# Kernel optimization log

Measured on AMD Instinct MI355X. Metric: run time of the kernel, lower is better.

The kernel has to match this reference:

```python
import jax, jax.numpy as jnp
import numpy as np

B, N_INST, C, K, H, W = 4, 64, 16, 4, 480, 480


def setup_inputs() -> dict:
    key = jax.random.key(0)
    k1, k2 = jax.random.split(key)
    # one binary-ish channel per instance, values in [0,1]
    update_map = jax.random.uniform(k1, (B, N_INST, H, W), dtype=jnp.float32)
    # current global instance-ID map, one channel per semantic category
    init_instance_map = jax.random.randint(k2, (B, C, H, W), 0, 50).astype(jnp.int32)
    # instance channel indices grouped by category (category c owns K instances)
    instance_ids = jnp.broadcast_to(
        jnp.arange(C * K, dtype=jnp.int32).reshape(C, K), (B, C, K)
    )
    return {
        "update_map": update_map,
        "init_instance_map": init_instance_map,
        "instance_ids": instance_ids,
    }


def reference(update_map, init_instance_map, instance_ids):
    b, n_inst, h, w = update_map.shape
    _, c, k = instance_ids.shape
    L = n_inst + 1  # local IDs live in [0, n_inst]
    BIG = jnp.int32(2 ** 30)

    # ---- aggregate instance channels per category (one-hot collapse) ----
    # gather the K instance channels of each category: [B, C, K, H, W]
    oh = jnp.take_along_axis(
        update_map[:, None, :, :, :],
        instance_ids[:, :, :, None, None].astype(jnp.int32),
        axis=2,
    )
    bg = jnp.full((b, c, 1, h, w), 1e-5, update_map.dtype)  # background plane
    idx = jnp.argmax(jnp.concatenate([bg, oh], axis=2), axis=2)  # [B, C, H, W]
    # remap argmax index -> instance ID via [0] + instance_ids
    padded_ids = jnp.concatenate(
        [jnp.zeros((b, c, 1), jnp.int32), instance_ids.astype(jnp.int32)], axis=2
    )  # [B, C, K+1]
    agg = padded_ids[
        jnp.arange(b)[:, None, None, None],
        jnp.arange(c)[None, :, None, None],
        idx,
    ]  # [B, C, H, W] local instance-ID map per category

    # ---- merge local IDs into global map, per env, sequential over categories ----
    def merge_env(gmap0, agg_e):
        def step(gmap, ci):
            local = agg_e[ci].reshape(-1)
            glob = gmap[ci].reshape(-1)
            max_id = jnp.max(gmap)  # max over ALL categories so far (sequential dep)
            # smallest overlapping nonzero global ID per local ID (torch.unique()[0])
            overlap_min = jax.ops.segment_min(
                jnp.where(glob != 0, glob, BIG), local, num_segments=L
            )
            present = jax.ops.segment_sum(
                jnp.ones_like(local), local, num_segments=L
            ) > 0
            has_overlap = overlap_min < BIG
            is_new = (present & (~has_overlap)).at[0].set(False)
            new_id = max_id + jnp.cumsum(is_new.astype(jnp.int32))
            mapping = jnp.where(has_overlap, overlap_min, jnp.where(is_new, new_id, 0))
            mapping = mapping.at[0].set(0)
            new_glob = jnp.maximum(glob, mapping[local]).reshape(h, w)
            updated = jnp.where(jnp.sum(agg_e[ci]) > 0, new_glob, gmap[ci])
            return gmap.at[ci].set(updated), None

        gmap, _ = jax.lax.scan(step, gmap0, jnp.arange(c))
        return gmap

    return jax.vmap(merge_env)(init_instance_map, agg)
```

## Files before the change

kernel.cpp:

```cpp
#include <hip/hip_runtime.h>
#include <stdint.h>
#include <limits.h>

#define BB 4
#define NI 64
#define CC 16
#define KK 4
#define HH 480
#define WW 480
#define PLANE (HH * WW)
#define NG (PLANE / 4)
#define BPP 45
#define GPT 5
#define TPB 256
#define BIGV (1 << 30)
#define NPLANE (BB * CC)

typedef float  v4f __attribute__((ext_vector_type(4)));
typedef int    v4i __attribute__((ext_vector_type(4)));

#define SEL8_BYTES ((size_t)NPLANE * PLANE)
#define PART_STRIDE 8
#define MAP_OFF (NPLANE * BPP * PART_STRIDE)

__device__ __forceinline__ int wred_min(int v) {
    for (int o = 32; o; o >>= 1) v = min(v, __shfl_down(v, o, 64));
    return v;
}
__device__ __forceinline__ int wred_max(int v) {
    for (int o = 32; o; o >>= 1) v = max(v, __shfl_down(v, o, 64));
    return v;
}
__device__ __forceinline__ int wred_or(int v) {
    for (int o = 32; o; o >>= 1) v |= __shfl_down(v, o, 64);
    return v;
}

__global__ __launch_bounds__(TPB) void stats_kernel(
    const float* __restrict__ update, const int* __restrict__ initmap,
    const int* __restrict__ inst_ids, unsigned int* __restrict__ sel8,
    int* __restrict__ wsi) {
    int plane = blockIdx.x / BPP;
    int chunk = blockIdx.x % BPP;
    int b = plane >> 4;

    int idbase = plane * KK;
    int id0 = inst_ids[idbase + 0], id1 = inst_ids[idbase + 1];
    int id2 = inst_ids[idbase + 2], id3 = inst_ids[idbase + 3];

    const v4f* u0 = (const v4f*)(update + ((size_t)b * NI + id0) * PLANE);
    const v4f* u1 = (const v4f*)(update + ((size_t)b * NI + id1) * PLANE);
    const v4f* u2 = (const v4f*)(update + ((size_t)b * NI + id2) * PLANE);
    const v4f* u3 = (const v4f*)(update + ((size_t)b * NI + id3) * PLANE);
    const v4i* gl = (const v4i*)(initmap + (size_t)plane * PLANE);
    unsigned int* sp = sel8 + (size_t)plane * NG;

    int lmin0 = INT_MAX, lmin1 = INT_MAX, lmin2 = INT_MAX, lmin3 = INT_MAX;
    int pres = 0, gmax = 0;

    int base = chunk * (TPB * GPT);
#pragma unroll
    for (int it = 0; it < GPT; it++) {
        int g = base + it * TPB + threadIdx.x;
        v4f a  = __builtin_nontemporal_load(&u0[g]);
        v4f b2 = __builtin_nontemporal_load(&u1[g]);
        v4f c  = __builtin_nontemporal_load(&u2[g]);
        v4f d  = __builtin_nontemporal_load(&u3[g]);
        v4i gv = __builtin_nontemporal_load(&gl[g]);

        unsigned int packed = 0;
#pragma unroll
        for (int e = 0; e < 4; e++) {
            float best = 1e-5f; int s = 0;
            if (a[e]  > best) { best = a[e];  s = 1; }
            if (b2[e] > best) { best = b2[e]; s = 2; }
            if (c[e]  > best) { best = c[e];  s = 3; }
            if (d[e]  > best) { s = 4; }
            int gve = gv[e];
            packed |= (unsigned int)(s * 50 + gve) << (8 * e);
            gmax = max(gmax, gve);
            if (s) {
                int kk = s - 1; pres |= 1 << kk;
                int v = gve ? gve : BIGV;
                if (kk == 0) lmin0 = min(lmin0, v);
                else if (kk == 1) lmin1 = min(lmin1, v);
                else if (kk == 2) lmin2 = min(lmin2, v);
                else lmin3 = min(lmin3, v);
            }
        }
        sp[g] = packed;
    }

    lmin0 = wred_min(lmin0); lmin1 = wred_min(lmin1);
    lmin2 = wred_min(lmin2); lmin3 = wred_min(lmin3);
    pres = wred_or(pres); gmax = wred_max(gmax);

    __shared__ int red[4][6];
    int wv = threadIdx.x >> 6, lane = threadIdx.x & 63;
    if (lane == 0) {
        red[wv][0] = lmin0; red[wv][1] = lmin1; red[wv][2] = lmin2;
        red[wv][3] = lmin3; red[wv][4] = pres;  red[wv][5] = gmax;
    }
    __syncthreads();
    if (threadIdx.x == 0) {
        int m0 = red[0][0], m1 = red[0][1], m2 = red[0][2], m3 = red[0][3];
        int pr = red[0][4], gm = red[0][5];
        for (int w2 = 1; w2 < 4; w2++) {
            m0 = min(m0, red[w2][0]); m1 = min(m1, red[w2][1]);
            m2 = min(m2, red[w2][2]); m3 = min(m3, red[w2][3]);
            pr |= red[w2][4]; gm = max(gm, red[w2][5]);
        }
        int* pp = wsi + ((size_t)plane * BPP + chunk) * PART_STRIDE;
        pp[0] = m0; pp[1] = m1; pp[2] = m2; pp[3] = m3; pp[4] = pr; pp[5] = gm;
    }
}

__global__ void mapping_kernel(const int* __restrict__ inst_ids, int* wsi) {
    __shared__ int s_ov[NPLANE][4];
    __shared__ int s_pr[NPLANE];
    __shared__ int s_gm[NPLANE];

    int plane = threadIdx.x;
    int m0 = INT_MAX, m1 = INT_MAX, m2 = INT_MAX, m3 = INT_MAX, pr = 0, gm = 0;
    for (int ch = 0; ch < BPP; ch++) {
        const int* pp = wsi + ((size_t)plane * BPP + ch) * PART_STRIDE;
        m0 = min(m0, pp[0]); m1 = min(m1, pp[1]);
        m2 = min(m2, pp[2]); m3 = min(m3, pp[3]);
        pr |= pp[4]; gm = max(gm, pp[5]);
    }
    s_ov[plane][0] = m0; s_ov[plane][1] = m1;
    s_ov[plane][2] = m2; s_ov[plane][3] = m3;
    s_pr[plane] = pr; s_gm[plane] = gm;
    __syncthreads();

    if (threadIdx.x < BB) {
        int b = threadIdx.x;
        int max_id = 0;
        for (int ci = 0; ci < CC; ci++) max_id = max(max_id, s_gm[b * CC + ci]);
        for (int ci = 0; ci < CC; ci++) {
            int pl = b * CC + ci;
            int base = pl * KK;
            int id[KK], ov[KK], prb[KK];
            int prbits = s_pr[pl];
            for (int t = 0; t < KK; t++) {
                id[t] = inst_ids[base + t];
                ov[t] = s_ov[pl][t];
                prb[t] = (prbits >> t) & 1;
            }
            int ord[KK] = {0, 1, 2, 3};
            for (int i = 1; i < KK; i++) {
                int key = ord[i], j = i - 1;
                while (j >= 0 && id[ord[j]] > id[key]) { ord[j + 1] = ord[j]; j--; }
                ord[j + 1] = key;
            }
            int map_slot[KK];
            int prev_id = -1, cur_map = 0, cnt_new = 0;
            for (int j = 0; j < KK; j++) {
                int s = ord[j], l = id[s];
                if (l != prev_id) {
                    int cov = INT_MAX, cpr = 0;
                    for (int t = 0; t < KK; t++)
                        if (id[t] == l) { cov = min(cov, ov[t]); cpr |= prb[t]; }
                    if (l == 0) cur_map = 0;
                    else {
                        bool has = cov < BIGV;
                        bool isnew = cpr && !has;
                        if (isnew) { cnt_new++; cur_map = max_id + cnt_new; }
                        else cur_map = has ? cov : 0;
                    }
                    prev_id = l;
                }
                map_slot[s] = cur_map;
            }
            for (int t = 0; t < KK; t++) wsi[MAP_OFF + base + t] = map_slot[t];
            max_id += cnt_new;
        }
    }
}

__global__ __launch_bounds__(TPB) void remap_kernel(
    const unsigned int* __restrict__ sel8, const int* __restrict__ wsi,
    int* __restrict__ out) {
    int plane = blockIdx.x / BPP;
    int chunk = blockIdx.x % BPP;

    int m0 = wsi[MAP_OFF + plane * 4 + 0];
    int m1 = wsi[MAP_OFF + plane * 4 + 1];
    int m2 = wsi[MAP_OFF + plane * 4 + 2];
    int m3 = wsi[MAP_OFF + plane * 4 + 3];

    const unsigned int* sp = sel8 + (size_t)plane * NG;
    v4i* op = (v4i*)(out + (size_t)plane * PLANE);

    int base = chunk * (TPB * GPT);
#pragma unroll
    for (int it = 0; it < GPT; it++) {
        int g = base + it * TPB + threadIdx.x;
        unsigned int u = sp[g];
        v4i ov;
#pragma unroll
        for (int e = 0; e < 4; e++) {
            unsigned int p = (u >> (8 * e)) & 0xFFu;
            int s = (int)((p * 41u) >> 11);
            int gvv = (int)p - s * 50;
            int mv = (s == 1) ? m0 : (s == 2) ? m1 : (s == 3) ? m2 : m3;
            ov[e] = s ? max(gvv, mv) : gvv;
        }
        __builtin_nontemporal_store(ov, &op[g]);
    }
}

extern "C" void kernel_launch(void* const* d_in, const int* in_sizes, int n_in,
                              void* d_out, int out_size, void* d_ws, size_t ws_size,
                              hipStream_t stream) {
    const float* update = (const float*)d_in[0];
    const int* initmap = (const int*)d_in[1];
    const int* inst_ids = (const int*)d_in[2];
    int* out = (int*)d_out;

    unsigned int* sel8 = (unsigned int*)d_ws;
    int* wsi = (int*)((uint8_t*)d_ws + SEL8_BYTES);

    stats_kernel<<<NPLANE * BPP, TPB, 0, stream>>>(update, initmap, inst_ids, sel8, wsi);
    mapping_kernel<<<1, NPLANE, 0, stream>>>(inst_ids, wsi);
    remap_kernel<<<NPLANE * BPP, TPB, 0, stream>>>(sel8, wsi, out);
}
```

Measured before the change: 388.1 us.

## Fuse stats, mapping and remap into one cooperative kernel with grid sync

Replaces the three-kernel pipeline with a single cooperative kernel. Each block keeps its packed selection/global bytes in registers, joins a grid-wide sync, and then redundantly computes the sequential per-batch mapping in its own shared memory before writing the output directly. This removes the sel8 intermediate write and re-read plus two kernel launches. In exchange the grid must be fully co-resident (1600 blocks, launch bounds raised to 8 blocks per CU), there is grid-sync overhead and redundant mapping work per block. The old three-kernel path is kept as a fallback if the cooperative launch fails.

```diff
diff --git a/kernel.cpp b/kernel.cpp
--- a/kernel.cpp
+++ b/kernel.cpp
@@ -1,6 +1,9 @@
 #include <hip/hip_runtime.h>
+#include <hip/hip_cooperative_groups.h>
 #include <stdint.h>
 #include <limits.h>
+
+namespace cg = cooperative_groups;
 
 #define BB 4
 #define NI 64
@@ -10,12 +13,16 @@
 #define WW 480
 #define PLANE (HH * WW)
 #define NG (PLANE / 4)
-#define BPP 45
-#define GPT 5
 #define TPB 256
 #define BIGV (1 << 30)
 #define NPLANE (BB * CC)
 
+#define FBPP 25
+#define FGPT 9
+
+#define BPP 45
+#define GPT 5
+
 typedef float  v4f __attribute__((ext_vector_type(4)));
 typedef int    v4i __attribute__((ext_vector_type(4)));
 
@@ -36,12 +43,13 @@
     return v;
 }
 
-__global__ __launch_bounds__(TPB) void stats_kernel(
+__global__ __launch_bounds__(TPB, 8) void fused_kernel(
     const float* __restrict__ update, const int* __restrict__ initmap,
-    const int* __restrict__ inst_ids, unsigned int* __restrict__ sel8,
+    const int* __restrict__ inst_ids, int* __restrict__ out,
     int* __restrict__ wsi) {
-    int plane = blockIdx.x / BPP;
-    int chunk = blockIdx.x % BPP;
+
+    int plane = blockIdx.x / FBPP;
+    int chunk = blockIdx.x % FBPP;
     int b = plane >> 4;
 
     int idbase = plane * KK;
@@ -53,14 +61,15 @@
     const v4f* u2 = (const v4f*)(update + ((size_t)b * NI + id2) * PLANE);
     const v4f* u3 = (const v4f*)(update + ((size_t)b * NI + id3) * PLANE);
     const v4i* gl = (const v4i*)(initmap + (size_t)plane * PLANE);
-    unsigned int* sp = sel8 + (size_t)plane * NG;
 
     int lmin0 = INT_MAX, lmin1 = INT_MAX, lmin2 = INT_MAX, lmin3 = INT_MAX;
     int pres = 0, gmax = 0;
 
-    int base = chunk * (TPB * GPT);
-#pragma unroll
-    for (int it = 0; it < GPT; it++) {
+    unsigned int held[FGPT];
+    int base = chunk * (TPB * FGPT);
+
+#pragma unroll
+    for (int it = 0; it < FGPT; it++) {
         int g = base + it * TPB + threadIdx.x;
         v4f a  = __builtin_nontemporal_load(&u0[g]);
         v4f b2 = __builtin_nontemporal_load(&u1[g]);
@@ -88,7 +97,7 @@
                 else lmin3 = min(lmin3, v);
             }
         }
-        sp[g] = packed;
+        held[it] = packed;
     }
 
     lmin0 = wred_min(lmin0); lmin1 = wred_min(lmin1);
@@ -96,6 +105,10 @@
     pres = wred_or(pres); gmax = wred_max(gmax);
 
     __shared__ int red[4][6];
+    __shared__ int s_red[CC][6];
+    __shared__ int s_ids[CC * KK];
+    __shared__ int s_map[KK];
+
     int wv = threadIdx.x >> 6, lane = threadIdx.x & 63;
     if (lane == 0) {
         red[wv][0] = lmin0; red[wv][1] = lmin1; red[wv][2] = lmin2;
@@ -110,41 +123,37 @@
             m2 = min(m2, red[w2][2]); m3 = min(m3, red[w2][3]);
             pr |= red[w2][4]; gm = max(gm, red[w2][5]);
         }
-        int* pp = wsi + ((size_t)plane * BPP + chunk) * PART_STRIDE;
+        int* pp = wsi + ((size_t)plane * FBPP + chunk) * PART_STRIDE;
         pp[0] = m0; pp[1] = m1; pp[2] = m2; pp[3] = m3; pp[4] = pr; pp[5] = gm;
     }
-}
-
-__global__ void mapping_kernel(const int* __restrict__ inst_ids, int* wsi) {
-    __shared__ int s_ov[NPLANE][4];
-    __shared__ int s_pr[NPLANE];
-    __shared__ int s_gm[NPLANE];
-
-    int plane = threadIdx.x;
-    int m0 = INT_MAX, m1 = INT_MAX, m2 = INT_MAX, m3 = INT_MAX, pr = 0, gm = 0;
-    for (int ch = 0; ch < BPP; ch++) {
-        const int* pp = wsi + ((size_t)plane * BPP + ch) * PART_STRIDE;
-        m0 = min(m0, pp[0]); m1 = min(m1, pp[1]);
-        m2 = min(m2, pp[2]); m3 = min(m3, pp[3]);
-        pr |= pp[4]; gm = max(gm, pp[5]);
-    }
-    s_ov[plane][0] = m0; s_ov[plane][1] = m1;
-    s_ov[plane][2] = m2; s_ov[plane][3] = m3;
-    s_pr[plane] = pr; s_gm[plane] = gm;
+
+    cg::this_grid().sync();
+
+    if (threadIdx.x < CC * KK) s_ids[threadIdx.x] = inst_ids[b * (CC * KK) + threadIdx.x];
+    if (threadIdx.x < CC * 6) {
+        int p16 = threadIdx.x / 6, slot = threadIdx.x % 6;
+        const int* rp = wsi + ((size_t)(b * CC + p16) * FBPP) * PART_STRIDE + slot;
+        int v = (slot < 4) ? INT_MAX : 0;
+        for (int ch = 0; ch < FBPP; ch++) {
+            int x = rp[ch * PART_STRIDE];
+            if (slot < 4)      v = min(v, x);
+            else if (slot == 4) v |= x;
+            else               v = max(v, x);
+        }
+        s_red[p16][slot] = v;
+    }
     __syncthreads();
 
-    if (threadIdx.x < BB) {
-        int b = threadIdx.x;
+    if (threadIdx.x == 0) {
         int max_id = 0;
-        for (int ci = 0; ci < CC; ci++) max_id = max(max_id, s_gm[b * CC + ci]);
-        for (int ci = 0; ci < CC; ci++) {
-            int pl = b * CC + ci;
-            int base = pl * KK;
+        for (int ci = 0; ci < CC; ci++) max_id = max(max_id, s_red[ci][5]);
+        int my_ci = plane & (CC - 1);
+        for (int ci = 0; ci <= my_ci; ci++) {
             int id[KK], ov[KK], prb[KK];
-            int prbits = s_pr[pl];
+            int prbits = s_red[ci][4];
             for (int t = 0; t < KK; t++) {
-                id[t] = inst_ids[base + t];
-                ov[t] = s_ov[pl][t];
+                id[t] = s_ids[ci * KK + t];
+                ov[t] = s_red[ci][t];
                 prb[t] = (prbits >> t) & 1;
             }
             int ord[KK] = {0, 1, 2, 3};
@@ -172,6 +181,171 @@
                 }
                 map_slot[s] = cur_map;
             }
+            if (ci == my_ci) {
+                s_map[0] = map_slot[0]; s_map[1] = map_slot[1];
+                s_map[2] = map_slot[2]; s_map[3] = map_slot[3];
+            }
+            max_id += cnt_new;
+        }
+    }
+    __syncthreads();
+
+    int m0 = s_map[0], m1 = s_map[1], m2 = s_map[2], m3 = s_map[3];
+
+    v4i* op = (v4i*)(out + (size_t)plane * PLANE);
+#pragma unroll
+    for (int it = 0; it < FGPT; it++) {
+        int g = base + it * TPB + threadIdx.x;
+        unsigned int u = held[it];
+        v4i ov;
+#pragma unroll
+        for (int e = 0; e < 4; e++) {
+            unsigned int p = (u >> (8 * e)) & 0xFFu;
+            int s = (int)((p * 41u) >> 11);
+            int gvv = (int)p - s * 50;
+            int mv = (s == 1) ? m0 : (s == 2) ? m1 : (s == 3) ? m2 : m3;
+            ov[e] = s ? max(gvv, mv) : gvv;
+        }
+        __builtin_nontemporal_store(ov, &op[g]);
+    }
+}
+
+__global__ __launch_bounds__(TPB) void stats_kernel(
+    const float* __restrict__ update, const int* __restrict__ initmap,
+    const int* __restrict__ inst_ids, unsigned int* __restrict__ sel8,
+    int* __restrict__ wsi) {
+    int plane = blockIdx.x / BPP;
+    int chunk = blockIdx.x % BPP;
+    int b = plane >> 4;
+
+    int idbase = plane * KK;
+    int id0 = inst_ids[idbase + 0], id1 = inst_ids[idbase + 1];
+    int id2 = inst_ids[idbase + 2], id3 = inst_ids[idbase + 3];
+
+    const v4f* u0 = (const v4f*)(update + ((size_t)b * NI + id0) * PLANE);
+    const v4f* u1 = (const v4f*)(update + ((size_t)b * NI + id1) * PLANE);
+    const v4f* u2 = (const v4f*)(update + ((size_t)b * NI + id2) * PLANE);
+    const v4f* u3 = (const v4f*)(update + ((size_t)b * NI + id3) * PLANE);
+    const v4i* gl = (const v4i*)(initmap + (size_t)plane * PLANE);
+    unsigned int* sp = sel8 + (size_t)plane * NG;
+
+    int lmin0 = INT_MAX, lmin1 = INT_MAX, lmin2 = INT_MAX, lmin3 = INT_MAX;
+    int pres = 0, gmax = 0;
+
+    int base = chunk * (TPB * GPT);
+#pragma unroll
+    for (int it = 0; it < GPT; it++) {
+        int g = base + it * TPB + threadIdx.x;
+        v4f a  = __builtin_nontemporal_load(&u0[g]);
+        v4f b2 = __builtin_nontemporal_load(&u1[g]);
+        v4f c  = __builtin_nontemporal_load(&u2[g]);
+        v4f d  = __builtin_nontemporal_load(&u3[g]);
+        v4i gv = __builtin_nontemporal_load(&gl[g]);
+
+        unsigned int packed = 0;
+#pragma unroll
+        for (int e = 0; e < 4; e++) {
+            float best = 1e-5f; int s = 0;
+            if (a[e]  > best) { best = a[e];  s = 1; }
+            if (b2[e] > best) { best = b2[e]; s = 2; }
+            if (c[e]  > best) { best = c[e];  s = 3; }
+            if (d[e]  > best) { s = 4; }
+            int gve = gv[e];
+            packed |= (unsigned int)(s * 50 + gve) << (8 * e);
+            gmax = max(gmax, gve);
+            if (s) {
+                int kk = s - 1; pres |= 1 << kk;
+                int v = gve ? gve : BIGV;
+                if (kk == 0) lmin0 = min(lmin0, v);
+                else if (kk == 1) lmin1 = min(lmin1, v);
+                else if (kk == 2) lmin2 = min(lmin2, v);
+                else lmin3 = min(lmin3, v);
+            }
+        }
+        sp[g] = packed;
+    }
+
+    lmin0 = wred_min(lmin0); lmin1 = wred_min(lmin1);
+    lmin2 = wred_min(lmin2); lmin3 = wred_min(lmin3);
+    pres = wred_or(pres); gmax = wred_max(gmax);
+
+    __shared__ int red[4][6];
+    int wv = threadIdx.x >> 6, lane = threadIdx.x & 63;
+    if (lane == 0) {
+        red[wv][0] = lmin0; red[wv][1] = lmin1; red[wv][2] = lmin2;
+        red[wv][3] = lmin3; red[wv][4] = pres;  red[wv][5] = gmax;
+    }
+    __syncthreads();
+    if (threadIdx.x == 0) {
+        int m0 = red[0][0], m1 = red[0][1], m2 = red[0][2], m3 = red[0][3];
+        int pr = red[0][4], gm = red[0][5];
+        for (int w2 = 1; w2 < 4; w2++) {
+            m0 = min(m0, red[w2][0]); m1 = min(m1, red[w2][1]);
+            m2 = min(m2, red[w2][2]); m3 = min(m3, red[w2][3]);
+            pr |= red[w2][4]; gm = max(gm, red[w2][5]);
+        }
+        int* pp = wsi + ((size_t)plane * BPP + chunk) * PART_STRIDE;
+        pp[0] = m0; pp[1] = m1; pp[2] = m2; pp[3] = m3; pp[4] = pr; pp[5] = gm;
+    }
+}
+
+__global__ void mapping_kernel(const int* __restrict__ inst_ids, int* wsi) {
+    __shared__ int s_ov[NPLANE][4];
+    __shared__ int s_pr[NPLANE];
+    __shared__ int s_gm[NPLANE];
+
+    int plane = threadIdx.x;
+    int m0 = INT_MAX, m1 = INT_MAX, m2 = INT_MAX, m3 = INT_MAX, pr = 0, gm = 0;
+    for (int ch = 0; ch < BPP; ch++) {
+        const int* pp = wsi + ((size_t)plane * BPP + ch) * PART_STRIDE;
+        m0 = min(m0, pp[0]); m1 = min(m1, pp[1]);
+        m2 = min(m2, pp[2]); m3 = min(m3, pp[3]);
+        pr |= pp[4]; gm = max(gm, pp[5]);
+    }
+    s_ov[plane][0] = m0; s_ov[plane][1] = m1;
+    s_ov[plane][2] = m2; s_ov[plane][3] = m3;
+    s_pr[plane] = pr; s_gm[plane] = gm;
+    __syncthreads();
+
+    if (threadIdx.x < BB) {
+        int b = threadIdx.x;
+        int max_id = 0;
+        for (int ci = 0; ci < CC; ci++) max_id = max(max_id, s_gm[b * CC + ci]);
+        for (int ci = 0; ci < CC; ci++) {
+            int pl = b * CC + ci;
+            int base = pl * KK;
+            int id[KK], ov[KK], prb[KK];
+            int prbits = s_pr[pl];
+            for (int t = 0; t < KK; t++) {
+                id[t] = inst_ids[base + t];
+                ov[t] = s_ov[pl][t];
+                prb[t] = (prbits >> t) & 1;
+            }
+            int ord[KK] = {0, 1, 2, 3};
+            for (int i = 1; i < KK; i++) {
+                int key = ord[i], j = i - 1;
+                while (j >= 0 && id[ord[j]] > id[key]) { ord[j + 1] = ord[j]; j--; }
+                ord[j + 1] = key;
+            }
+            int map_slot[KK];
+            int prev_id = -1, cur_map = 0, cnt_new = 0;
+            for (int j = 0; j < KK; j++) {
+                int s = ord[j], l = id[s];
+                if (l != prev_id) {
+                    int cov = INT_MAX, cpr = 0;
+                    for (int t = 0; t < KK; t++)
+                        if (id[t] == l) { cov = min(cov, ov[t]); cpr |= prb[t]; }
+                    if (l == 0) cur_map = 0;
+                    else {
+                        bool has = cov < BIGV;
+                        bool isnew = cpr && !has;
+                        if (isnew) { cnt_new++; cur_map = max_id + cnt_new; }
+                        else cur_map = has ? cov : 0;
+                    }
+                    prev_id = l;
+                }
+                map_slot[s] = cur_map;
+            }
             for (int t = 0; t < KK; t++) wsi[MAP_OFF + base + t] = map_slot[t];
             max_id += cnt_new;
         }
@@ -218,10 +392,19 @@
     const int* inst_ids = (const int*)d_in[2];
     int* out = (int*)d_out;
 
-    unsigned int* sel8 = (unsigned int*)d_ws;
-    int* wsi = (int*)((uint8_t*)d_ws + SEL8_BYTES);
-
-    stats_kernel<<<NPLANE * BPP, TPB, 0, stream>>>(update, initmap, inst_ids, sel8, wsi);
-    mapping_kernel<<<1, NPLANE, 0, stream>>>(inst_ids, wsi);
-    remap_kernel<<<NPLANE * BPP, TPB, 0, stream>>>(sel8, wsi, out);
-}
+    int* wsi_fused = (int*)d_ws;
+    void* args[] = { (void*)&update, (void*)&initmap, (void*)&inst_ids,
+                     (void*)&out, (void*)&wsi_fused };
+    hipError_t e = hipLaunchCooperativeKernel(
+        (const void*)fused_kernel, dim3(NPLANE * FBPP), dim3(TPB),
+        args, 0, stream);
+
+    if (e != hipSuccess) {
+        (void)hipGetLastError();
+        unsigned int* sel8 = (unsigned int*)d_ws;
+        int* wsi = (int*)((uint8_t*)d_ws + SEL8_BYTES);
+        stats_kernel<<<NPLANE * BPP, TPB, 0, stream>>>(update, initmap, inst_ids, sel8, wsi);
+        mapping_kernel<<<1, NPLANE, 0, stream>>>(inst_ids, wsi);
+        remap_kernel<<<NPLANE * BPP, TPB, 0, stream>>>(sel8, wsi, out);
+    }
+}
```

Result: slower. 637.8 us (+64.3%).

## Fold single-block mapping kernel into remap kernel, recomputing mapping per block

Applied to the files above, without the earlier changes.

Removes the separate one-block mapping kernel. Each remap block now reduces the per-chunk partial statistics for its batch's 16 planes, then runs the sequential category mapping up to its own plane in thread 0. It also issues the sel8 loads before this work so memory latency overlaps the mapping computation. This saves a kernel launch and a serialized single-block step, at the cost of redundant reduction and mapping work in every one of the 2880 blocks.

```diff
diff --git a/kernel.cpp b/kernel.cpp
--- a/kernel.cpp
+++ b/kernel.cpp
@@ -15,13 +15,13 @@
 #define TPB 256
 #define BIGV (1 << 30)
 #define NPLANE (BB * CC)
+#define NBLK (NPLANE * BPP)
 
 typedef float  v4f __attribute__((ext_vector_type(4)));
 typedef int    v4i __attribute__((ext_vector_type(4)));
 
 #define SEL8_BYTES ((size_t)NPLANE * PLANE)
 #define PART_STRIDE 8
-#define MAP_OFF (NPLANE * BPP * PART_STRIDE)
 
 __device__ __forceinline__ int wred_min(int v) {
     for (int o = 32; o; o >>= 1) v = min(v, __shfl_down(v, o, 64));
@@ -115,36 +115,52 @@
     }
 }
 
-__global__ void mapping_kernel(const int* __restrict__ inst_ids, int* wsi) {
-    __shared__ int s_ov[NPLANE][4];
-    __shared__ int s_pr[NPLANE];
-    __shared__ int s_gm[NPLANE];
-
-    int plane = threadIdx.x;
-    int m0 = INT_MAX, m1 = INT_MAX, m2 = INT_MAX, m3 = INT_MAX, pr = 0, gm = 0;
-    for (int ch = 0; ch < BPP; ch++) {
-        const int* pp = wsi + ((size_t)plane * BPP + ch) * PART_STRIDE;
-        m0 = min(m0, pp[0]); m1 = min(m1, pp[1]);
-        m2 = min(m2, pp[2]); m3 = min(m3, pp[3]);
-        pr |= pp[4]; gm = max(gm, pp[5]);
-    }
-    s_ov[plane][0] = m0; s_ov[plane][1] = m1;
-    s_ov[plane][2] = m2; s_ov[plane][3] = m3;
-    s_pr[plane] = pr; s_gm[plane] = gm;
+__global__ __launch_bounds__(TPB) void remap_map_kernel(
+    const unsigned int* __restrict__ sel8, const int* __restrict__ inst_ids,
+    const int* __restrict__ wsi, int* __restrict__ out) {
+
+    __shared__ int s_red[CC][6];
+    __shared__ int s_ids[CC * KK];
+    __shared__ int s_map[KK];
+
+    int plane = blockIdx.x / BPP;
+    int chunk = blockIdx.x % BPP;
+    int b = plane >> 4;
+
+    const unsigned int* sp = sel8 + (size_t)plane * NG;
+    int base = chunk * (TPB * GPT);
+
+    unsigned int u0 = sp[base + 0 * TPB + threadIdx.x];
+    unsigned int u1 = sp[base + 1 * TPB + threadIdx.x];
+    unsigned int u2 = sp[base + 2 * TPB + threadIdx.x];
+    unsigned int u3 = sp[base + 3 * TPB + threadIdx.x];
+    unsigned int u4 = sp[base + 4 * TPB + threadIdx.x];
+
+    if (threadIdx.x < CC * KK) s_ids[threadIdx.x] = inst_ids[b * (CC * KK) + threadIdx.x];
+    if (threadIdx.x < CC * 6) {
+        int p16 = threadIdx.x / 6, slot = threadIdx.x % 6;
+        const int* rp = wsi + ((size_t)(b * CC + p16) * BPP) * PART_STRIDE + slot;
+        int v = (slot < 4) ? INT_MAX : 0;
+        for (int ch = 0; ch < BPP; ch++) {
+            int x = rp[ch * PART_STRIDE];
+            if (slot < 4)      v = min(v, x);
+            else if (slot == 4) v |= x;
+            else               v = max(v, x);
+        }
+        s_red[p16][slot] = v;
+    }
     __syncthreads();
 
-    if (threadIdx.x < BB) {
-        int b = threadIdx.x;
+    if (threadIdx.x == 0) {
         int max_id = 0;
-        for (int ci = 0; ci < CC; ci++) max_id = max(max_id, s_gm[b * CC + ci]);
-        for (int ci = 0; ci < CC; ci++) {
-            int pl = b * CC + ci;
-            int base = pl * KK;
+        for (int ci = 0; ci < CC; ci++) max_id = max(max_id, s_red[ci][5]);
+        int my_ci = plane & (CC - 1);
+        for (int ci = 0; ci <= my_ci; ci++) {
             int id[KK], ov[KK], prb[KK];
-            int prbits = s_pr[pl];
+            int prbits = s_red[ci][4];
             for (int t = 0; t < KK; t++) {
-                id[t] = inst_ids[base + t];
-                ov[t] = s_ov[pl][t];
+                id[t] = s_ids[ci * KK + t];
+                ov[t] = s_red[ci][t];
                 prb[t] = (prbits >> t) & 1;
             }
             int ord[KK] = {0, 1, 2, 3};
@@ -172,31 +188,23 @@
                 }
                 map_slot[s] = cur_map;
             }
-            for (int t = 0; t < KK; t++) wsi[MAP_OFF + base + t] = map_slot[t];
+            if (ci == my_ci) {
+                s_map[0] = map_slot[0]; s_map[1] = map_slot[1];
+                s_map[2] = map_slot[2]; s_map[3] = map_slot[3];
+            }
             max_id += cnt_new;
         }
     }
-}
-
-__global__ __launch_bounds__(TPB) void remap_kernel(
-    const unsigned int* __restrict__ sel8, const int* __restrict__ wsi,
-    int* __restrict__ out) {
-    int plane = blockIdx.x / BPP;
-    int chunk = blockIdx.x % BPP;
-
-    int m0 = wsi[MAP_OFF + plane * 4 + 0];
-    int m1 = wsi[MAP_OFF + plane * 4 + 1];
-    int m2 = wsi[MAP_OFF + plane * 4 + 2];
-    int m3 = wsi[MAP_OFF + plane * 4 + 3];
-
-    const unsigned int* sp = sel8 + (size_t)plane * NG;
+    __syncthreads();
+
+    int m0 = s_map[0], m1 = s_map[1], m2 = s_map[2], m3 = s_map[3];
+
     v4i* op = (v4i*)(out + (size_t)plane * PLANE);
-
-    int base = chunk * (TPB * GPT);
+    unsigned int uu[GPT] = {u0, u1, u2, u3, u4};
 #pragma unroll
     for (int it = 0; it < GPT; it++) {
         int g = base + it * TPB + threadIdx.x;
-        unsigned int u = sp[g];
+        unsigned int u = uu[it];
         v4i ov;
 #pragma unroll
         for (int e = 0; e < 4; e++) {
@@ -221,7 +229,6 @@
     unsigned int* sel8 = (unsigned int*)d_ws;
     int* wsi = (int*)((uint8_t*)d_ws + SEL8_BYTES);
 
-    stats_kernel<<<NPLANE * BPP, TPB, 0, stream>>>(update, initmap, inst_ids, sel8, wsi);
-    mapping_kernel<<<1, NPLANE, 0, stream>>>(inst_ids, wsi);
-    remap_kernel<<<NPLANE * BPP, TPB, 0, stream>>>(sel8, wsi, out);
-}
+    stats_kernel<<<NBLK, TPB, 0, stream>>>(update, initmap, inst_ids, sel8, wsi);
+    remap_map_kernel<<<NBLK, TPB, 0, stream>>>(sel8, inst_ids, wsi, out);
+}
```

New measurement: 413.1 us. 1.06x slower.
